# Kernel tuning notes

Measured on AMD Instinct MI355X. Metric: run time of the kernel, lower is better.

Reference implementation:

```python
import jax, jax.numpy as jnp
import numpy as np

N = 500
PX = 1e-6
WAVELENGTH = 0.561e-6
FOCAL = 6e-3
LASER_FWHC = 2e-4
N_REFR = 1.33
K = 2.0 * N_REFR * np.pi / WAVELENGTH          # wavenumber
MAX_INTENSITY = 50000.0
UNIF_BG = 100.0
NOISE_MEAN = 3e8
NOISE_STD = 2e8
MAX_VAL = 4e9
PATCH = 31                                      # PSF patch is 31x31


def _constants():
    x = np.arange(-N // 2, N // 2)
    X, Y = np.meshgrid(x, x)
    X = X * PX; Y = Y * PX
    C1 = (np.pi / (WAVELENGTH * FOCAL) * (X ** 2 + Y ** 2)) % (2 * np.pi)
    B1 = np.exp(-1j * C1).astype(np.complex64)
    mask_real = np.exp(-(X ** 2 + Y ** 2) / (2 * LASER_FWHC ** 2)).astype(np.float32)
    xx = np.arange(-N + 1, N + 1)
    XX, YY = np.meshgrid(xx, xx)
    XX = XX * PX; YY = YY * PX
    Q1 = np.exp(1j * (np.pi * N_REFR / (WAVELENGTH * FOCAL)) * (XX ** 2 + YY ** 2)).astype(np.complex64)
    Fs = 1.0 / PX
    F = np.arange(-Fs / 2, Fs / 2, Fs / N)
    alpha = N_REFR * WAVELENGTH * F
    A, B = np.meshgrid(alpha, alpha)
    gamma = np.sqrt(1.0 - A ** 2 - B ** 2).astype(np.float32)
    return B1, mask_real, Q1, gamma


def setup_inputs() -> dict:
    key = jax.random.key(0)
    k1, k2, k3, k4, k5, k6, k7 = jax.random.split(key, 7)
    B1, mask_real, Q1, gamma = _constants()
    Bsz, E = 2, 64
    mask_param = jax.random.normal(k1, (N, N), jnp.float32)
    xy = jax.random.randint(k2, (Bsz, E, 2), 15, 185)       # patch centers inside 200x200 canvas
    z = jax.random.randint(k3, (Bsz, E, 1), 0, 31)          # defocus index, 31 PSF planes
    xyz = jnp.concatenate([xy, z], axis=-1).astype(jnp.int32)
    nphotons = jax.random.uniform(k4, (Bsz, E), jnp.float32)  # unused by forward (as in source)
    psf_imgs = jax.random.uniform(k5, (31, PATCH, PATCH), jnp.float32)  # stand-in for beads_img_defocus tiffs
    noise_gauss = jax.random.normal(k6, (Bsz, 1, 200, 200), jnp.float32)
    noise_poiss = jax.random.normal(k7, (Bsz, 1, 200, 200), jnp.float32)
    return {
        "mask_param": mask_param, "xyz": xyz, "nphotons": nphotons,
        "B1": jnp.asarray(B1), "Q1": jnp.asarray(Q1),
        "mask_real": jnp.asarray(mask_real), "gamma_cust": jnp.asarray(gamma),
        "psf_imgs": psf_imgs, "noise_gauss": noise_gauss, "noise_poiss": noise_poiss,
    }


def _forward(mask_param, xyz, nphotons, B1, Q1, mask_real, gamma_cust,
             psf_imgs, noise_gauss, noise_poiss):
    Bsz, E, _ = xyz.shape
    # phase mask applied to laser beam profile
    M = mask_real * jnp.exp(1j * mask_param)                 # (N,N) complex
    field = B1 * M
    E1 = jnp.pad(field, ((250, 250), (250, 250)))            # (2N,2N)
    E2 = jnp.fft.ifftshift(jnp.fft.ifft2(jnp.fft.fft2(E1) * jnp.fft.fft2(Q1)))
    out = E2[N // 2:3 * N // 2, N // 2:3 * N // 2]           # (N,N) complex
    Fout = jnp.fft.fftshift(jnp.fft.fft2(out))               # shared spectrum

    xs = (xyz[..., 0] - 100).reshape(-1).astype(jnp.float32)  # per-emitter defocus distance
    zs = xyz[..., 2].reshape(-1)

    def emitter_intensity(xf, zi):
        phase = jnp.exp(1j * (K * 1e-6) * gamma_cust * xf)
        U = jnp.fft.ifft2(jnp.fft.ifftshift(Fout * phase))
        I = jnp.real(U * jnp.conj(U))                        # (N,N)
        col = jax.lax.dynamic_slice_in_dim(I, 249 + zi, 1, axis=1)
        return jnp.sum(col)

    intens = jax.vmap(emitter_intensity)(xs, zs).reshape(Bsz, E)

    # per-emitter 31x31 PSF patch scaled by intensity, scatter-added onto 200x200 canvas
    patches = psf_imgs[jnp.abs(xyz[..., 2])] * intens[..., None, None]  # (B,E,31,31)
    d = jnp.arange(-15, 16)
    rows = xyz[..., 0][..., None] + d                        # (B,E,31)
    cols = xyz[..., 1][..., None] + d
    bidx = jnp.arange(Bsz)[:, None, None, None]
    canvas = jnp.zeros((Bsz, 200, 200), jnp.float32)
    canvas = canvas.at[bidx, rows[:, :, :, None], cols[:, :, None, :]].add(patches)
    imgs3D = canvas[:, None] / MAX_INTENSITY                 # (B,1,200,200)

    # NoiseLayer: uniform bg + gaussian-approximated poisson noise
    inp = imgs3D + UNIF_BG
    inp = inp + 1e5 + (NOISE_STD * noise_gauss + NOISE_MEAN)
    inp = jnp.where(inp <= 0, 0.0, inp)
    noisy = inp + 100.0 * jnp.sqrt(inp) * noise_poiss

    # Normalize01
    noisy = jnp.where(noisy <= 10.0, 1.0, noisy)
    noisy = jnp.minimum(noisy, MAX_VAL)
    return noisy / MAX_VAL


def reference(mask_param, xyz, nphotons, B1, Q1, mask_real, gamma_cust,
              psf_imgs, noise_gauss, noise_poiss):
    return _forward(mask_param, xyz, nphotons, B1, Q1, mask_real, gamma_cust,
                    psf_imgs, noise_gauss, noise_poiss)
```

## Files before the change

### kernel.cpp

```cpp
#include <hip/hip_runtime.h>
#include <math.h>


__device__ __forceinline__ float2 cmulf(float2 a, float2 b) {
  return make_float2(a.x * b.x - a.y * b.y, a.x * b.y + a.y * b.x);
}

template <int N>
__device__ __forceinline__ void build_tw_lds(float2* tw, int tid, int nthr) {
  const float inv = 1.0f / (float)N;
  for (int k = tid; k < N; k += nthr) {
    float fr = (float)k * inv;
    tw[k] = make_float2(__builtin_amdgcn_cosf(fr),
                        -__builtin_amdgcn_sinf(fr));
  }
}

template <int NFFT, int INV>
__device__ __forceinline__ float2* fft_core_g(float2* X, float2* Y,
                                              const float2* tw, int tid,
                                              int tstride, int twstride) {
  int Ns = 1;
  const int NF = (NFFT == 1000) ? 6 : 5;
  const int N2 = (NFFT == 1000) ? 3 : 2;
  const float W5r[5] = {1.f, 0.30901699f, -0.80901699f, -0.80901699f,
                        0.30901699f};
  const float W5i[5] = {0.f, INV ? 0.95105652f : -0.95105652f,
                        INV ? 0.58778525f : -0.58778525f,
                        INV ? -0.58778525f : 0.58778525f,
                        INV ? -0.95105652f : 0.95105652f};
  for (int p = 0; p < NF; ++p) {
    const int R = (p < N2) ? 2 : 5;
    const int NR = NFFT / R;
    const int stepk = NFFT / (Ns * R);
    for (int j = tid; j < NR; j += tstride) {
      const int jm = j % Ns;
      const int jd = j / Ns;
      const int idxD = jd * (Ns * R) + jm;
      if (R == 2) {
        float2 v0 = X[j];
        float2 w = tw[jm * stepk * twstride];
        if (INV) w.y = -w.y;
        float2 v1 = cmulf(X[j + NR], w);
        Y[idxD] = make_float2(v0.x + v1.x, v0.y + v1.y);
        Y[idxD + Ns] = make_float2(v0.x - v1.x, v0.y - v1.y);
      } else {
        float2 v[5];
        v[0] = X[j];
#pragma unroll
        for (int s = 1; s < 5; ++s) {
          float2 w = tw[jm * s * stepk * twstride];
          if (INV) w.y = -w.y;
          v[s] = cmulf(X[j + s * NR], w);
        }
#pragma unroll
        for (int t5 = 0; t5 < 5; ++t5) {
          float ax = v[0].x, ay = v[0].y;
#pragma unroll
          for (int s = 1; s < 5; ++s) {
            const int m = (s * t5) % 5;
            ax += v[s].x * W5r[m] - v[s].y * W5i[m];
            ay += v[s].x * W5i[m] + v[s].y * W5r[m];
          }
          Y[idxD + t5 * Ns] = make_float2(ax, ay);
        }
      }
    }
    __syncthreads();
    float2* t = X;
    X = Y;
    Y = t;
    Ns *= R;
  }
  return X;
}

__global__ __launch_bounds__(256) void e1_fft_kernel(
    const float* __restrict__ mask_param, const float* __restrict__ mask_real,
    float2* __restrict__ A, float2* __restrict__ qv) {
  __shared__ float2 bufA[1000];
  __shared__ float2 bufB[1000];
  __shared__ float2 twl[1000];
  const int b = blockIdx.x;
  const int tid = threadIdx.x;
  build_tw_lds<1000>(twl, tid, 256);
  if (b == 500) {
    for (int i = tid; i < 1000; i += 256) {
      double xv = (double)(i - 499) * 1e-6;
      const double s2rev = 1.33 / (2.0 * 5.61e-7 * 0.006);
      double t = s2rev * xv * xv;
      float fr = (float)(t - floor(t));
      bufA[i] =
          make_float2(__builtin_amdgcn_cosf(fr), __builtin_amdgcn_sinf(fr));
    }
    __syncthreads();
    float2* X = fft_core_g<1000, 0>(bufA, bufB, twl, tid, 256, 1);
    for (int i = tid; i < 1000; i += 256) qv[i] = X[i];
    return;
  }
  const int rm = b;
  for (int i = tid; i < 1000; i += 256) {
    float2 val = make_float2(0.f, 0.f);
    if (i >= 250 && i < 750) {
      int cm = i - 250;
      int p = rm * 500 + cm;
      double xv = (double)(cm - 250) * 1e-6;
      double yv = (double)(rm - 250) * 1e-6;
      const double s1rev = 1.0 / (2.0 * 5.61e-7 * 0.006);
      double t = s1rev * (xv * xv + yv * yv);
      float fr = (float)(t - floor(t));
      float cb = __builtin_amdgcn_cosf(fr);
      float sb = __builtin_amdgcn_sinf(fr);
      float th = mask_param[p];
      float s, co;
      __sincosf(th, &s, &co);
      float m = mask_real[p];
      val = make_float2(m * (cb * co + sb * s), m * (cb * s - sb * co));
    }
    bufA[i] = val;
  }
  __syncthreads();
  float2* X = fft_core_g<1000, 0>(bufA, bufB, twl, tid, 256, 1);
  float2* dst = A + (size_t)(rm + 250) * 1000;
  for (int i = tid; i < 1000; i += 256) dst[i] = X[i];
}

__global__ __launch_bounds__(256) void colmul1000_kernel(
    float2* A, const float2* __restrict__ qv) {
  __shared__ float2 bufA[1000];
  __shared__ float2 bufB[1000];
  __shared__ float2 twl[1000];
  const int tid = threadIdx.x;
  const int b = blockIdx.x;
  const int c = (b & 7) * 125 + (b >> 3);
  build_tw_lds<1000>(twl, tid, 256);
  for (int r = tid; r < 1000; r += 256) {
    float2 v = make_float2(0.f, 0.f);
    if (r >= 250 && r < 750) v = A[(size_t)r * 1000 + c];
    bufA[r] = v;
  }
  __syncthreads();
  float2* X = fft_core_g<1000, 0>(bufA, bufB, twl, tid, 256, 1);
  float2 qc = qv[c];
  qc.x *= 1e-6f;
  qc.y *= 1e-6f;
  for (int j = tid; j < 1000; j += 256) X[j] = cmulf(X[j], cmulf(qc, qv[j]));
  __syncthreads();
  float2* Y = (X == bufA) ? bufB : bufA;
  float2* Z = fft_core_g<1000, 1>(X, Y, twl, tid, 256, 1);
  for (int r = tid; r < 1000; r += 256) {
    if (r < 250 || r >= 750) A[(size_t)r * 1000 + c] = Z[r];
  }
}

__global__ __launch_bounds__(256) void ifft_crop_fft500_kernel(
    const float2* __restrict__ A, float2* __restrict__ C5) {
  __shared__ float2 bufA[1000];
  __shared__ float2 bufB[1000];
  __shared__ float2 twl[1000];
  const int r = blockIdx.x;
  const int rr = (750 + r) % 1000;
  const int tid = threadIdx.x;
  build_tw_lds<1000>(twl, tid, 256);
  const float2* src = A + (size_t)rr * 1000;
  for (int i = tid; i < 1000; i += 256) bufA[i] = src[i];
  __syncthreads();
  float2* X = fft_core_g<1000, 1>(bufA, bufB, twl, tid, 256, 1);
  float2* Y = (X == bufA) ? bufB : bufA;
  for (int c = tid; c < 500; c += 256) {
    int cc = (c < 250) ? (750 + c) : (c - 250);
    Y[c] = X[cc];
  }
  __syncthreads();
  float2* Z = fft_core_g<500, 0>(Y, X, twl, tid, 256, 2);
  float2* dst = C5 + (size_t)r * 500;
  for (int i = tid; i < 500; i += 256) dst[i] = Z[i];
}

__global__ __launch_bounds__(256) void col500_fout_kernel(
    const float2* __restrict__ C5, float2* __restrict__ Fout,
    float* __restrict__ canvas) {
  __shared__ float2 cA[2000];
  __shared__ float2 cB[2000];
  __shared__ float2 twl[500];
  const int bid = blockIdx.x;
  const int tid = threadIdx.x;
  if (bid >= 125) {
    int i = (bid - 125) * 256 + tid;
    if (i < 80000) canvas[i] = 0.f;
    return;
  }
  const int cl = tid >> 6, lane = tid & 63;
  const int c0 = bid * 4;
  build_tw_lds<500>(twl, tid, 256);
  for (int idx = tid; idx < 2000; idx += 256) {
    int r = idx >> 2, cc = idx & 3;
    cA[cc * 500 + r] = C5[(size_t)r * 500 + c0 + cc];
  }
  __syncthreads();
  fft_core_g<500, 0>(cA + cl * 500, cB + cl * 500, twl, lane, 64,
                     1);
  for (int idx = tid; idx < 2000; idx += 256) {
    int u = idx >> 2, cc = idx & 3;
    int v = (c0 + cc + 250) % 500;
    Fout[(size_t)u * 500 + v] = cB[cc * 500 + (u + 250) % 500];
  }
}

__global__ void fill_out_kernel(float* __restrict__ out, int n) {
  int i = blockIdx.x * blockDim.x + threadIdx.x;
  if (i < n) out[i] = 0.f;
}

__global__ __launch_bounds__(64) void emitter_partial_kernel(
    const float2* __restrict__ Fout, const float* __restrict__ gamma,
    const int* __restrict__ xyz, float* __restrict__ partial) {
  const int u = blockIdx.x;
  const int eg = blockIdx.y;
  const int lane = threadIdx.x;
  const float krev = 2.37076648841354f;
  const float2* Frow = Fout + u * 500;
  const float* grow = gamma + u * 500;
  float fx[8], fy[8], gg[8];
#pragma unroll
  for (int k = 0; k < 8; ++k) {
    int v = lane + 64 * k;
    if (v < 500) {
      float2 F = Frow[v];
      fx[k] = F.x;
      fy[k] = F.y;
      gg[k] = grow[v];
    } else {
      fx[k] = 0.f;
      fy[k] = 0.f;
      gg[k] = 0.f;
    }
  }
#pragma unroll 1
  for (int i = 0; i < 16; ++i) {
    const int e = eg * 16 + i;
    const float xf = (float)(xyz[e * 3 + 0] - 100);
    const int zc = 249 + xyz[e * 3 + 2];
    const float gx = krev * xf;
    int m = (zc * lane) % 500;
    const int step = (zc * 64) % 500;
    float ax = 0.f, ay = 0.f;
#pragma unroll
    for (int k = 0; k < 8; ++k) {
      float rev = fmaf(gx, gg[k], (float)m * 0.002f);
      float r = rev - floorf(rev);
      float s = __builtin_amdgcn_sinf(r);
      float co = __builtin_amdgcn_cosf(r);
      ax += fx[k] * co - fy[k] * s;
      ay += fx[k] * s + fy[k] * co;
      m += step;
      if (m >= 500) m -= 500;
    }
#pragma unroll
    for (int off = 1; off < 64; off <<= 1) {
      ax += __shfl_xor(ax, off, 64);
      ay += __shfl_xor(ay, off, 64);
    }
    if (lane == 0) partial[e * 500 + u] = (ax * ax + ay * ay) * 8.0e-9f;
  }
}

__global__ __launch_bounds__(256) void emitter_reduce_scatter_kernel(
    const float* __restrict__ partial, const float* __restrict__ psf,
    const int* __restrict__ xyz, float* __restrict__ canvas) {
  const int e = blockIdx.x;
  const int tid = threadIdx.x;
  __shared__ float red[4];
  float s = 0.f;
  for (int k = tid; k < 500; k += 256) s += partial[e * 500 + k];
#pragma unroll
  for (int off = 1; off < 64; off <<= 1) s += __shfl_xor(s, off, 64);
  if ((tid & 63) == 0) red[tid >> 6] = s;
  __syncthreads();
  const float inten = red[0] + red[1] + red[2] + red[3];
  const int x = xyz[e * 3 + 0];
  const int y = xyz[e * 3 + 1];
  const int z = xyz[e * 3 + 2];
  const int zz = (z < 0) ? -z : z;
  const int b = e >> 6;
  for (int t = tid; t < 961; t += 256) {
    int i = t / 31, j = t % 31;
    atomicAdd(&canvas[b * 40000 + (x - 15 + i) * 200 + (y - 15 + j)],
              psf[zz * 961 + t] * inten);
  }
}

__global__ void final_kernel(const float* __restrict__ canvas,
                             const float* __restrict__ ng,
                             const float* __restrict__ npz,
                             float* __restrict__ out) {
  int idx = blockIdx.x * blockDim.x + threadIdx.x;
  if (idx >= 80000) return;
  float inp = canvas[idx] / 50000.0f + 100.0f;
  inp = inp + 100000.0f + (2.0e8f * ng[idx] + 3.0e8f);
  if (inp <= 0.0f) inp = 0.0f;
  float noisy = inp + 100.0f * sqrtf(inp) * npz[idx];
  noisy = (noisy <= 10.0f) ? 1.0f : noisy;
  noisy = fminf(noisy, 4.0e9f);
  out[idx] = noisy / 4.0e9f;
}

extern "C" void kernel_launch(void* const* d_in, const int* in_sizes, int n_in,
                              void* d_out, int out_size, void* d_ws,
                              size_t ws_size, hipStream_t stream) {
  const float* mask_param = (const float*)d_in[0];
  const int* xyz = (const int*)d_in[1];
  const float* mask_real = (const float*)d_in[5];
  const float* gamma = (const float*)d_in[6];
  const float* psf = (const float*)d_in[7];
  const float* ng = (const float*)d_in[8];
  const float* npz = (const float*)d_in[9];
  float* out = (float*)d_out;

  char* p = (char*)d_ws;
  auto carve = [&](size_t bytes) -> char* {
    char* r = p;
    p += (bytes + 255) & ~(size_t)255;
    return r;
  };
  float2* A = (float2*)carve(1000 * 1000 * sizeof(float2));
  float2* C5 = (float2*)carve(500 * 500 * sizeof(float2));
  float2* Fn = (float2*)carve(500 * 500 * sizeof(float2));
  float* partial = (float*)carve(128 * 500 * sizeof(float));
  float2* qv = (float2*)carve(1000 * sizeof(float2));
  float* canvas = (float*)carve(80000 * sizeof(float));
  size_t need = (size_t)(p - (char*)d_ws);
  if (ws_size < need) {
    fill_out_kernel<<<(out_size + 255) / 256, 256, 0, stream>>>(out, out_size);
    return;
  }

  e1_fft_kernel<<<501, 256, 0, stream>>>(mask_param, mask_real, A, qv);
  colmul1000_kernel<<<1000, 256, 0, stream>>>(A, qv);
  ifft_crop_fft500_kernel<<<500, 256, 0, stream>>>(A, C5);
  col500_fout_kernel<<<438, 256, 0, stream>>>(C5, Fn, canvas);

  dim3 eg(500, 8);
  emitter_partial_kernel<<<eg, 64, 0, stream>>>(Fn, gamma, xyz, partial);
  emitter_reduce_scatter_kernel<<<128, 256, 0, stream>>>(partial, psf, xyz,
                                                         canvas);
  final_kernel<<<313, 256, 0, stream>>>(canvas, ng, npz, out);
}
```

Before: 152.3 us.

## Fuse pipeline into a single cooperative persistent kernel with grid syncs

Replaces the seven separate kernel launches with one cooperative mega-kernel of 512 persistent blocks. Stages are separated by grid.sync(), and the twiddle table is built once per block instead of once per stage. The aim is to remove launch gaps and repeated twiddle setup. In exchange, each stage runs with at most 512 blocks, and 40KB of LDS per block may cap occupancy. Grid-wide barriers add their own cost, and stages with fewer items (125, 128) leave most blocks idle.

```diff
diff --git a/kernel.cpp b/kernel.cpp
--- a/kernel.cpp
+++ b/kernel.cpp
@@ -1,19 +1,12 @@
 #include <hip/hip_runtime.h>
+#include <hip/hip_cooperative_groups.h>
 #include <math.h>
+
+namespace cg = cooperative_groups;
 
 
 __device__ __forceinline__ float2 cmulf(float2 a, float2 b) {
   return make_float2(a.x * b.x - a.y * b.y, a.x * b.y + a.y * b.x);
-}
-
-template <int N>
-__device__ __forceinline__ void build_tw_lds(float2* tw, int tid, int nthr) {
-  const float inv = 1.0f / (float)N;
-  for (int k = tid; k < N; k += nthr) {
-    float fr = (float)k * inv;
-    tw[k] = make_float2(__builtin_amdgcn_cosf(fr),
-                        -__builtin_amdgcn_sinf(fr));
-  }
 }
 
 template <int NFFT, int INV>
@@ -75,234 +68,233 @@
   return X;
 }
 
-__global__ __launch_bounds__(256) void e1_fft_kernel(
+__global__ __launch_bounds__(256, 2) void mega_kernel(
     const float* __restrict__ mask_param, const float* __restrict__ mask_real,
-    float2* __restrict__ A, float2* __restrict__ qv) {
-  __shared__ float2 bufA[1000];
-  __shared__ float2 bufB[1000];
-  __shared__ float2 twl[1000];
-  const int b = blockIdx.x;
+    const int* __restrict__ xyz, const float* __restrict__ gamma,
+    const float* __restrict__ psf, const float* __restrict__ ng,
+    const float* __restrict__ npz, float2* __restrict__ A,
+    float2* __restrict__ C5, float2* __restrict__ Fn,
+    float* __restrict__ partial, float2* __restrict__ qv,
+    float* __restrict__ canvas, float* __restrict__ out) {
+  cg::grid_group grid = cg::this_grid();
+  __shared__ float2 smem[5000];
+  float2* twl = smem;
+  float2* buf = smem + 1000;
+  float2* bufA = buf;
+  float2* bufB = buf + 1000;
   const int tid = threadIdx.x;
-  build_tw_lds<1000>(twl, tid, 256);
-  if (b == 500) {
-    for (int i = tid; i < 1000; i += 256) {
-      double xv = (double)(i - 499) * 1e-6;
-      const double s2rev = 1.33 / (2.0 * 5.61e-7 * 0.006);
-      double t = s2rev * xv * xv;
-      float fr = (float)(t - floor(t));
-      bufA[i] =
-          make_float2(__builtin_amdgcn_cosf(fr), __builtin_amdgcn_sinf(fr));
+
+  for (int k = tid; k < 1000; k += 256) {
+    float fr = (float)k * 0.001f;
+    twl[k] =
+        make_float2(__builtin_amdgcn_cosf(fr), -__builtin_amdgcn_sinf(fr));
+  }
+  __syncthreads();
+
+  for (int b = blockIdx.x; b <= 500; b += gridDim.x) {
+    if (b == 500) {
+      for (int i = tid; i < 1000; i += 256) {
+        double xv = (double)(i - 499) * 1e-6;
+        const double s2rev = 1.33 / (2.0 * 5.61e-7 * 0.006);
+        double t = s2rev * xv * xv;
+        float fr = (float)(t - floor(t));
+        bufA[i] =
+            make_float2(__builtin_amdgcn_cosf(fr), __builtin_amdgcn_sinf(fr));
+      }
+    } else {
+      const int rm = b;
+      for (int i = tid; i < 1000; i += 256) {
+        float2 val = make_float2(0.f, 0.f);
+        if (i >= 250 && i < 750) {
+          int cm = i - 250;
+          int p = rm * 500 + cm;
+          double xv = (double)(cm - 250) * 1e-6;
+          double yv = (double)(rm - 250) * 1e-6;
+          const double s1rev = 1.0 / (2.0 * 5.61e-7 * 0.006);
+          double t = s1rev * (xv * xv + yv * yv);
+          float fr = (float)(t - floor(t));
+          float cb = __builtin_amdgcn_cosf(fr);
+          float sb = __builtin_amdgcn_sinf(fr);
+          float th = mask_param[p];
+          float s, co;
+          __sincosf(th, &s, &co);
+          float m = mask_real[p];
+          val = make_float2(m * (cb * co + sb * s), m * (cb * s - sb * co));
+        }
+        bufA[i] = val;
+      }
     }
     __syncthreads();
     float2* X = fft_core_g<1000, 0>(bufA, bufB, twl, tid, 256, 1);
-    for (int i = tid; i < 1000; i += 256) qv[i] = X[i];
-    return;
-  }
-  const int rm = b;
-  for (int i = tid; i < 1000; i += 256) {
-    float2 val = make_float2(0.f, 0.f);
-    if (i >= 250 && i < 750) {
-      int cm = i - 250;
-      int p = rm * 500 + cm;
-      double xv = (double)(cm - 250) * 1e-6;
-      double yv = (double)(rm - 250) * 1e-6;
-      const double s1rev = 1.0 / (2.0 * 5.61e-7 * 0.006);
-      double t = s1rev * (xv * xv + yv * yv);
-      float fr = (float)(t - floor(t));
-      float cb = __builtin_amdgcn_cosf(fr);
-      float sb = __builtin_amdgcn_sinf(fr);
-      float th = mask_param[p];
-      float s, co;
-      __sincosf(th, &s, &co);
-      float m = mask_real[p];
-      val = make_float2(m * (cb * co + sb * s), m * (cb * s - sb * co));
-    }
-    bufA[i] = val;
-  }
-  __syncthreads();
-  float2* X = fft_core_g<1000, 0>(bufA, bufB, twl, tid, 256, 1);
-  float2* dst = A + (size_t)(rm + 250) * 1000;
-  for (int i = tid; i < 1000; i += 256) dst[i] = X[i];
-}
-
-__global__ __launch_bounds__(256) void colmul1000_kernel(
-    float2* A, const float2* __restrict__ qv) {
-  __shared__ float2 bufA[1000];
-  __shared__ float2 bufB[1000];
-  __shared__ float2 twl[1000];
-  const int tid = threadIdx.x;
-  const int b = blockIdx.x;
-  const int c = (b & 7) * 125 + (b >> 3);
-  build_tw_lds<1000>(twl, tid, 256);
-  for (int r = tid; r < 1000; r += 256) {
-    float2 v = make_float2(0.f, 0.f);
-    if (r >= 250 && r < 750) v = A[(size_t)r * 1000 + c];
-    bufA[r] = v;
-  }
-  __syncthreads();
-  float2* X = fft_core_g<1000, 0>(bufA, bufB, twl, tid, 256, 1);
-  float2 qc = qv[c];
-  qc.x *= 1e-6f;
-  qc.y *= 1e-6f;
-  for (int j = tid; j < 1000; j += 256) X[j] = cmulf(X[j], cmulf(qc, qv[j]));
-  __syncthreads();
-  float2* Y = (X == bufA) ? bufB : bufA;
-  float2* Z = fft_core_g<1000, 1>(X, Y, twl, tid, 256, 1);
-  for (int r = tid; r < 1000; r += 256) {
-    if (r < 250 || r >= 750) A[(size_t)r * 1000 + c] = Z[r];
-  }
-}
-
-__global__ __launch_bounds__(256) void ifft_crop_fft500_kernel(
-    const float2* __restrict__ A, float2* __restrict__ C5) {
-  __shared__ float2 bufA[1000];
-  __shared__ float2 bufB[1000];
-  __shared__ float2 twl[1000];
-  const int r = blockIdx.x;
-  const int rr = (750 + r) % 1000;
-  const int tid = threadIdx.x;
-  build_tw_lds<1000>(twl, tid, 256);
-  const float2* src = A + (size_t)rr * 1000;
-  for (int i = tid; i < 1000; i += 256) bufA[i] = src[i];
-  __syncthreads();
-  float2* X = fft_core_g<1000, 1>(bufA, bufB, twl, tid, 256, 1);
-  float2* Y = (X == bufA) ? bufB : bufA;
-  for (int c = tid; c < 500; c += 256) {
-    int cc = (c < 250) ? (750 + c) : (c - 250);
-    Y[c] = X[cc];
-  }
-  __syncthreads();
-  float2* Z = fft_core_g<500, 0>(Y, X, twl, tid, 256, 2);
-  float2* dst = C5 + (size_t)r * 500;
-  for (int i = tid; i < 500; i += 256) dst[i] = Z[i];
-}
-
-__global__ __launch_bounds__(256) void col500_fout_kernel(
-    const float2* __restrict__ C5, float2* __restrict__ Fout,
-    float* __restrict__ canvas) {
-  __shared__ float2 cA[2000];
-  __shared__ float2 cB[2000];
-  __shared__ float2 twl[500];
-  const int bid = blockIdx.x;
-  const int tid = threadIdx.x;
-  if (bid >= 125) {
-    int i = (bid - 125) * 256 + tid;
-    if (i < 80000) canvas[i] = 0.f;
-    return;
-  }
-  const int cl = tid >> 6, lane = tid & 63;
-  const int c0 = bid * 4;
-  build_tw_lds<500>(twl, tid, 256);
-  for (int idx = tid; idx < 2000; idx += 256) {
-    int r = idx >> 2, cc = idx & 3;
-    cA[cc * 500 + r] = C5[(size_t)r * 500 + c0 + cc];
-  }
-  __syncthreads();
-  fft_core_g<500, 0>(cA + cl * 500, cB + cl * 500, twl, lane, 64,
-                     1);
-  for (int idx = tid; idx < 2000; idx += 256) {
-    int u = idx >> 2, cc = idx & 3;
-    int v = (c0 + cc + 250) % 500;
-    Fout[(size_t)u * 500 + v] = cB[cc * 500 + (u + 250) % 500];
+    if (b == 500) {
+      for (int i = tid; i < 1000; i += 256) qv[i] = X[i];
+    } else {
+      float2* dst = A + (size_t)(b + 250) * 1000;
+      for (int i = tid; i < 1000; i += 256) dst[i] = X[i];
+    }
+    __syncthreads();
+  }
+  grid.sync();
+
+  for (int b = blockIdx.x; b < 1000; b += gridDim.x) {
+    const int c = (b & 7) * 125 + (b >> 3);
+    for (int r = tid; r < 1000; r += 256) {
+      float2 v = make_float2(0.f, 0.f);
+      if (r >= 250 && r < 750) v = A[(size_t)r * 1000 + c];
+      bufA[r] = v;
+    }
+    __syncthreads();
+    float2* X = fft_core_g<1000, 0>(bufA, bufB, twl, tid, 256, 1);
+    float2 qc = qv[c];
+    qc.x *= 1e-6f;
+    qc.y *= 1e-6f;
+    for (int j = tid; j < 1000; j += 256) X[j] = cmulf(X[j], cmulf(qc, qv[j]));
+    __syncthreads();
+    float2* Y = (X == bufA) ? bufB : bufA;
+    float2* Z = fft_core_g<1000, 1>(X, Y, twl, tid, 256, 1);
+    for (int r = tid; r < 1000; r += 256)
+      if (r < 250 || r >= 750) A[(size_t)r * 1000 + c] = Z[r];
+    __syncthreads();
+  }
+  grid.sync();
+
+  for (int b = blockIdx.x; b < 500; b += gridDim.x) {
+    const int rr = (750 + b) % 1000;
+    const float2* src = A + (size_t)rr * 1000;
+    for (int i = tid; i < 1000; i += 256) bufA[i] = src[i];
+    __syncthreads();
+    float2* X = fft_core_g<1000, 1>(bufA, bufB, twl, tid, 256, 1);
+    float2* Y = (X == bufA) ? bufB : bufA;
+    for (int ci = tid; ci < 500; ci += 256) {
+      int cc = (ci < 250) ? (750 + ci) : (ci - 250);
+      Y[ci] = X[cc];
+    }
+    __syncthreads();
+    float2* Z = fft_core_g<500, 0>(Y, X, twl, tid, 256, 2);
+    float2* dst = C5 + (size_t)b * 500;
+    for (int i = tid; i < 500; i += 256) dst[i] = Z[i];
+    __syncthreads();
+  }
+  grid.sync();
+
+  for (int i = blockIdx.x * 256 + tid; i < 80000; i += gridDim.x * 256)
+    canvas[i] = 0.f;
+  {
+    const int cl = tid >> 6, lane = tid & 63;
+    float2* cA = buf;
+    float2* cB = buf + 2000;
+    for (int b = blockIdx.x; b < 125; b += gridDim.x) {
+      const int c0 = b * 4;
+      for (int idx = tid; idx < 2000; idx += 256) {
+        int r = idx >> 2, cc = idx & 3;
+        cA[cc * 500 + r] = C5[(size_t)r * 500 + c0 + cc];
+      }
+      __syncthreads();
+      fft_core_g<500, 0>(cA + cl * 500, cB + cl * 500, twl, lane, 64, 2);
+      for (int idx = tid; idx < 2000; idx += 256) {
+        int u = idx >> 2, cc = idx & 3;
+        int v = (c0 + cc + 250) % 500;
+        Fn[(size_t)u * 500 + v] = cB[cc * 500 + (u + 250) % 500];
+      }
+      __syncthreads();
+    }
+  }
+  grid.sync();
+
+  {
+    const int lane = tid & 63;
+    const int nw = gridDim.x * 4;
+    const float krev = 2.37076648841354f;
+    for (int t = blockIdx.x * 4 + (tid >> 6); t < 4000; t += nw) {
+      const int u = t >> 3;
+      const int eg = t & 7;
+      const float2* Frow = Fn + u * 500;
+      const float* grow = gamma + u * 500;
+      float fx[8], fy[8], gg[8];
+#pragma unroll
+      for (int k = 0; k < 8; ++k) {
+        int v = lane + 64 * k;
+        if (v < 500) {
+          float2 F = Frow[v];
+          fx[k] = F.x;
+          fy[k] = F.y;
+          gg[k] = grow[v];
+        } else {
+          fx[k] = 0.f;
+          fy[k] = 0.f;
+          gg[k] = 0.f;
+        }
+      }
+#pragma unroll 1
+      for (int i = 0; i < 16; ++i) {
+        const int e = eg * 16 + i;
+        const float xf = (float)(xyz[e * 3 + 0] - 100);
+        const int zc = 249 + xyz[e * 3 + 2];
+        const float gx = krev * xf;
+        int m = (zc * lane) % 500;
+        const int step = (zc * 64) % 500;
+        float ax = 0.f, ay = 0.f;
+#pragma unroll
+        for (int k = 0; k < 8; ++k) {
+          float rev = fmaf(gx, gg[k], (float)m * 0.002f);
+          float r = rev - floorf(rev);
+          float s = __builtin_amdgcn_sinf(r);
+          float co = __builtin_amdgcn_cosf(r);
+          ax += fx[k] * co - fy[k] * s;
+          ay += fx[k] * s + fy[k] * co;
+          m += step;
+          if (m >= 500) m -= 500;
+        }
+#pragma unroll
+        for (int off = 1; off < 64; off <<= 1) {
+          ax += __shfl_xor(ax, off, 64);
+          ay += __shfl_xor(ay, off, 64);
+        }
+        if (lane == 0) partial[e * 500 + u] = (ax * ax + ay * ay) * 8.0e-9f;
+      }
+    }
+  }
+  grid.sync();
+
+  {
+    float* redf = (float*)buf;
+    for (int e = blockIdx.x; e < 128; e += gridDim.x) {
+      float s = 0.f;
+      for (int k = tid; k < 500; k += 256) s += partial[e * 500 + k];
+#pragma unroll
+      for (int off = 1; off < 64; off <<= 1) s += __shfl_xor(s, off, 64);
+      if ((tid & 63) == 0) redf[tid >> 6] = s;
+      __syncthreads();
+      const float inten = redf[0] + redf[1] + redf[2] + redf[3];
+      const int x = xyz[e * 3 + 0];
+      const int y = xyz[e * 3 + 1];
+      const int z = xyz[e * 3 + 2];
+      const int zz = (z < 0) ? -z : z;
+      const int b = e >> 6;
+      for (int t = tid; t < 961; t += 256) {
+        int i = t / 31, j = t % 31;
+        atomicAdd(&canvas[b * 40000 + (x - 15 + i) * 200 + (y - 15 + j)],
+                  psf[zz * 961 + t] * inten);
+      }
+      __syncthreads();
+    }
+  }
+  grid.sync();
+
+  for (int idx = blockIdx.x * 256 + tid; idx < 80000; idx += gridDim.x * 256) {
+    float inp = canvas[idx] / 50000.0f + 100.0f;
+    inp = inp + 100000.0f + (2.0e8f * ng[idx] + 3.0e8f);
+    if (inp <= 0.0f) inp = 0.0f;
+    float noisy = inp + 100.0f * sqrtf(inp) * npz[idx];
+    noisy = (noisy <= 10.0f) ? 1.0f : noisy;
+    noisy = fminf(noisy, 4.0e9f);
+    out[idx] = noisy / 4.0e9f;
   }
 }
 
 __global__ void fill_out_kernel(float* __restrict__ out, int n) {
   int i = blockIdx.x * blockDim.x + threadIdx.x;
   if (i < n) out[i] = 0.f;
-}
-
-__global__ __launch_bounds__(64) void emitter_partial_kernel(
-    const float2* __restrict__ Fout, const float* __restrict__ gamma,
-    const int* __restrict__ xyz, float* __restrict__ partial) {
-  const int u = blockIdx.x;
-  const int eg = blockIdx.y;
-  const int lane = threadIdx.x;
-  const float krev = 2.37076648841354f;
-  const float2* Frow = Fout + u * 500;
-  const float* grow = gamma + u * 500;
-  float fx[8], fy[8], gg[8];
-#pragma unroll
-  for (int k = 0; k < 8; ++k) {
-    int v = lane + 64 * k;
-    if (v < 500) {
-      float2 F = Frow[v];
-      fx[k] = F.x;
-      fy[k] = F.y;
-      gg[k] = grow[v];
-    } else {
-      fx[k] = 0.f;
-      fy[k] = 0.f;
-      gg[k] = 0.f;
-    }
-  }
-#pragma unroll 1
-  for (int i = 0; i < 16; ++i) {
-    const int e = eg * 16 + i;
-    const float xf = (float)(xyz[e * 3 + 0] - 100);
-    const int zc = 249 + xyz[e * 3 + 2];
-    const float gx = krev * xf;
-    int m = (zc * lane) % 500;
-    const int step = (zc * 64) % 500;
-    float ax = 0.f, ay = 0.f;
-#pragma unroll
-    for (int k = 0; k < 8; ++k) {
-      float rev = fmaf(gx, gg[k], (float)m * 0.002f);
-      float r = rev - floorf(rev);
-      float s = __builtin_amdgcn_sinf(r);
-      float co = __builtin_amdgcn_cosf(r);
-      ax += fx[k] * co - fy[k] * s;
-      ay += fx[k] * s + fy[k] * co;
-      m += step;
-      if (m >= 500) m -= 500;
-    }
-#pragma unroll
-    for (int off = 1; off < 64; off <<= 1) {
-      ax += __shfl_xor(ax, off, 64);
-      ay += __shfl_xor(ay, off, 64);
-    }
-    if (lane == 0) partial[e * 500 + u] = (ax * ax + ay * ay) * 8.0e-9f;
-  }
-}
-
-__global__ __launch_bounds__(256) void emitter_reduce_scatter_kernel(
-    const float* __restrict__ partial, const float* __restrict__ psf,
-    const int* __restrict__ xyz, float* __restrict__ canvas) {
-  const int e = blockIdx.x;
-  const int tid = threadIdx.x;
-  __shared__ float red[4];
-  float s = 0.f;
-  for (int k = tid; k < 500; k += 256) s += partial[e * 500 + k];
-#pragma unroll
-  for (int off = 1; off < 64; off <<= 1) s += __shfl_xor(s, off, 64);
-  if ((tid & 63) == 0) red[tid >> 6] = s;
-  __syncthreads();
-  const float inten = red[0] + red[1] + red[2] + red[3];
-  const int x = xyz[e * 3 + 0];
-  const int y = xyz[e * 3 + 1];
-  const int z = xyz[e * 3 + 2];
-  const int zz = (z < 0) ? -z : z;
-  const int b = e >> 6;
-  for (int t = tid; t < 961; t += 256) {
-    int i = t / 31, j = t % 31;
-    atomicAdd(&canvas[b * 40000 + (x - 15 + i) * 200 + (y - 15 + j)],
-              psf[zz * 961 + t] * inten);
-  }
-}
-
-__global__ void final_kernel(const float* __restrict__ canvas,
-                             const float* __restrict__ ng,
-                             const float* __restrict__ npz,
-                             float* __restrict__ out) {
-  int idx = blockIdx.x * blockDim.x + threadIdx.x;
-  if (idx >= 80000) return;
-  float inp = canvas[idx] / 50000.0f + 100.0f;
-  inp = inp + 100000.0f + (2.0e8f * ng[idx] + 3.0e8f);
-  if (inp <= 0.0f) inp = 0.0f;
-  float noisy = inp + 100.0f * sqrtf(inp) * npz[idx];
-  noisy = (noisy <= 10.0f) ? 1.0f : noisy;
-  noisy = fminf(noisy, 4.0e9f);
-  out[idx] = noisy / 4.0e9f;
 }
 
 extern "C" void kernel_launch(void* const* d_in, const int* in_sizes, int n_in,
@@ -335,14 +327,9 @@
     return;
   }
 
-  e1_fft_kernel<<<501, 256, 0, stream>>>(mask_param, mask_real, A, qv);
-  colmul1000_kernel<<<1000, 256, 0, stream>>>(A, qv);
-  ifft_crop_fft500_kernel<<<500, 256, 0, stream>>>(A, C5);
-  col500_fout_kernel<<<438, 256, 0, stream>>>(C5, Fn, canvas);
-
-  dim3 eg(500, 8);
-  emitter_partial_kernel<<<eg, 64, 0, stream>>>(Fn, gamma, xyz, partial);
-  emitter_reduce_scatter_kernel<<<128, 256, 0, stream>>>(partial, psf, xyz,
-                                                         canvas);
-  final_kernel<<<313, 256, 0, stream>>>(canvas, ng, npz, out);
-}
+  void* args[] = {&mask_param, &mask_real, &xyz, &gamma, &psf,
+                  &ng,         &npz,       &A,   &C5,    &Fn,
+                  &partial,    &qv,        &canvas, &out};
+  hipLaunchCooperativeKernel((void*)mega_kernel, dim3(512), dim3(256), args,
+                             0, stream);
+}
```

Result: slower. 479.4 us (+214.7%).
